# Performance work log

Hardware: AMD Instinct MI355X
Metric: run time of the kernel (lower is better)

## Reference

```python
import jax, jax.numpy as jnp
import numpy as np

N_ENT = 50000
N_REL = 200
DIM = 128
N_BASES = 4
NUM_RELATIONS = 2 * N_REL  # RGCNConv num_relations
E = 200000
S = 20000


def rgcn_conv(x, edge_index, edge_type, edge_norm, basis, att, root, bias, n_nodes):
    """RGCNConv with basis decomposition, aggr='mean'.
    x: [N, Din]; basis: [B, Din, Dout]; att: [R, B]; root: [Din, Dout]; bias: [Dout].
    """
    src, dst = edge_index[0], edge_index[1]
    x_j = x[src]                      # [E, Din] gather
    att_e = att[edge_type]            # [E, B]
    # message: x_j @ (att_e @ basis) without materializing per-edge [Din,Dout] weights
    msg = jnp.einsum('ei,bio,eb->eo', x_j, basis, att_e)  # [E, Dout]
    msg = msg * edge_norm[:, None]
    agg = jax.ops.segment_sum(msg, dst, num_segments=n_nodes)            # [N, Dout]
    cnt = jax.ops.segment_sum(jnp.ones_like(edge_norm), dst, num_segments=n_nodes)
    agg = agg / jnp.maximum(cnt, 1.0)[:, None]            # mean aggregation
    return agg + x @ root + bias


def setup_inputs() -> dict:
    key = jax.random.key(0)
    ks = jax.random.split(key, 20)
    d = {}
    d['entity'] = jnp.arange(N_ENT, dtype=jnp.int64) if jax.config.read('jax_enable_x64') else jnp.arange(N_ENT, dtype=jnp.int32)
    d['edge_index'] = jax.random.randint(ks[0], (2, E), 0, N_ENT)
    d['edge_type'] = jax.random.randint(ks[1], (E,), 0, NUM_RELATIONS)
    d['edge_norm'] = jax.random.uniform(ks[2], (E,), dtype=jnp.float32)
    d['samples'] = jax.random.randint(ks[3], (S, 3), 0, N_REL)
    d['DAD_rel'] = jax.random.normal(ks[4], (N_REL, N_REL), dtype=jnp.float32) * 0.05
    # learned parameters
    d['entity_emb'] = jax.random.normal(ks[5], (N_ENT, DIM), dtype=jnp.float32) * 0.02
    d['relation_emb'] = jax.random.normal(ks[6], (N_REL, DIM), dtype=jnp.float32) * 0.02
    d['entity_context_tab'] = jax.random.normal(ks[7], (N_ENT, DIM), dtype=jnp.float32) * 0.02
    d['relation_context_tab'] = jax.random.normal(ks[8], (N_REL, DIM), dtype=jnp.float32) * 0.02
    d['relation_gcn_weight'] = jax.random.normal(ks[9], (DIM, DIM), dtype=jnp.float32) * 0.02
    d['gate_entity'] = jax.random.uniform(ks[10], (DIM,), dtype=jnp.float32)
    d['gate_relation'] = jax.random.uniform(ks[11], (DIM,), dtype=jnp.float32)
    d['basis1'] = jax.random.normal(ks[12], (N_BASES, DIM, DIM), dtype=jnp.float32) * 0.02
    d['att1'] = jax.random.normal(ks[13], (NUM_RELATIONS, N_BASES), dtype=jnp.float32) * 0.1
    d['root1'] = jax.random.normal(ks[14], (DIM, DIM), dtype=jnp.float32) * 0.02
    d['bias1'] = jnp.zeros((DIM,), dtype=jnp.float32)
    d['basis2'] = jax.random.normal(ks[15], (N_BASES, DIM, DIM), dtype=jnp.float32) * 0.02
    d['att2'] = jax.random.normal(ks[16], (NUM_RELATIONS, N_BASES), dtype=jnp.float32) * 0.1
    d['root2'] = jax.random.normal(ks[17], (DIM, DIM), dtype=jnp.float32) * 0.02
    d['bias2'] = jnp.zeros((DIM,), dtype=jnp.float32)
    return d


def reference(entity, edge_index, edge_type, edge_norm, samples, DAD_rel,
              entity_emb, relation_emb, entity_context_tab, relation_context_tab,
              relation_gcn_weight, gate_entity, gate_relation,
              basis1, att1, root1, bias1, basis2, att2, root2, bias2):
    n_nodes = entity.shape[0]
    ent_ctx = entity_context_tab[entity]                  # [N, D]
    rel_ctx = relation_context_tab                        # arange over all relations -> full table
    ent_ctx = jax.nn.relu(rgcn_conv(ent_ctx, edge_index, edge_type, edge_norm,
                                    basis1, att1, root1, bias1, n_nodes))
    ent_ctx = jax.nn.relu(rgcn_conv(ent_ctx, edge_index, edge_type, edge_norm,
                                    basis2, att2, root2, bias2, n_nodes))
    rel_ctx = jax.nn.relu((DAD_rel @ rel_ctx) @ relation_gcn_weight)
    ge = jax.nn.sigmoid(gate_entity)
    gr = jax.nn.sigmoid(gate_relation)
    h, r, t = samples[:, 0], samples[:, 1], samples[:, 2]
    head_o = ge * entity_emb[h] + (1.0 - ge) * ent_ctx[h]
    rel_o = gr * relation_emb[r] + (1.0 - gr) * rel_ctx[r]
    tail_o = ge * entity_emb[t] + (1.0 - ge) * ent_ctx[t]
    return jnp.stack([head_o, rel_o, tail_o])             # [3, S, D]
```

## Files before the change

kernel.cpp:

```cpp
#include <hip/hip_runtime.h>
#include <hip/hip_bf16.h>

typedef short s8v  __attribute__((ext_vector_type(8)));
typedef float f16v __attribute__((ext_vector_type(16)));

__device__ __forceinline__ unsigned short f2bf(float x) {
    unsigned u = __float_as_uint(x);
    unsigned r = ((u >> 16) & 1u) + 0x7FFFu;
    return (unsigned short)((u + r) >> 16);
}
__device__ __forceinline__ float bf2f(unsigned short h) {
    return __uint_as_float(((unsigned)h) << 16);
}

__global__ __launch_bounds__(256) void x0_kernel(
    const float* __restrict__ tab, const int* __restrict__ entity,
    float* __restrict__ X0, int N)
{
    int idx = blockIdx.x * 256 + threadIdx.x;
    int n = idx >> 5, l = idx & 31;
    if (n < N) {
        int src = entity[n];
        *(float4*)&X0[(size_t)n * 128 + l * 4] =
            *(const float4*)&tab[(size_t)src * 128 + l * 4];
    }
}

__global__ __launch_bounds__(256) void bprep_kernel(
    const float* __restrict__ basis1, const float* __restrict__ root1,
    const float* __restrict__ basis2, const float* __restrict__ root2,
    unsigned short* __restrict__ Bp1h, unsigned short* __restrict__ Bp1l,
    unsigned short* __restrict__ Bp2h, unsigned short* __restrict__ Bp2l)
{
    int idx = blockIdx.x * 256 + threadIdx.x;
    int layer = blockIdx.y;
    int n = idx & 127, k = idx >> 7;
    const float* basis = layer ? basis2 : basis1;
    const float* root  = layer ? root2  : root1;
    float v = (k < 512) ? basis[((k & 3) << 14) + ((k >> 2) << 7) + n]
                        : root[((k - 512) << 7) + n];
    unsigned short h = f2bf(v);
    unsigned short l = f2bf(v - bf2f(h));
    size_t pos = (((size_t)(k >> 3) * 128) + n) * 8 + (k & 7);
    unsigned short* Bh = layer ? Bp2h : Bp1h;
    unsigned short* Bl = layer ? Bp2l : Bp1l;
    Bh[pos] = h;
    Bl[pos] = l;
}

__global__ __launch_bounds__(256) void hist_kernel(
    const int* __restrict__ edge_index, int* __restrict__ deg, int E)
{
    int e = blockIdx.x * 256 + threadIdx.x;
    if (e < E) atomicAdd(&deg[edge_index[E + e]], 1);
}

__global__ __launch_bounds__(1024) void scanA_kernel(
    const int* __restrict__ deg, int* __restrict__ row_start,
    int* __restrict__ btot, int N)
{
    __shared__ int wtot[16];
    __shared__ int woff[16];
    const int tid = threadIdx.x, lane = tid & 63, wid = tid >> 6;
    int i = blockIdx.x * 1024 + tid;
    int v = (i < N) ? deg[i] : 0;
    int x = v;
    #pragma unroll
    for (int d = 1; d < 64; d <<= 1) {
        int t = __shfl_up(x, d, 64);
        if (lane >= d) x += t;
    }
    if (lane == 63) wtot[wid] = x;
    __syncthreads();
    if (wid == 0 && lane < 16) {
        int s = wtot[lane];
        int y = s;
        #pragma unroll
        for (int d = 1; d < 16; d <<= 1) {
            int t = __shfl_up(y, d, 16);
            if (lane >= d) y += t;
        }
        woff[lane] = y - s;
        if (lane == 15) btot[blockIdx.x] = y;
    }
    __syncthreads();
    if (i < N) row_start[i] = woff[wid] + (x - v);
}

__global__ __launch_bounds__(64) void scanB_kernel(
    const int* __restrict__ btot, int* __restrict__ boff,
    int* __restrict__ row_start, int nB, int N)
{
    int t = threadIdx.x;
    int v = (t < nB) ? btot[t] : 0;
    int x = v;
    #pragma unroll
    for (int d = 1; d < 64; d <<= 1) {
        int u = __shfl_up(x, d, 64);
        if (t >= d) x += u;
    }
    if (t < nB) boff[t] = x - v;
    if (t == nB - 1) row_start[N] = x;
}

__global__ __launch_bounds__(1024) void scanC_kernel(
    int* __restrict__ row_start, int* __restrict__ cursor,
    const int* __restrict__ boff, int N)
{
    int i = blockIdx.x * 1024 + threadIdx.x;
    if (i < N) {
        int r = row_start[i] + boff[blockIdx.x];
        row_start[i] = r;
        cursor[i]    = r;
    }
}

__global__ __launch_bounds__(256) void fill_kernel(
    const int* __restrict__ edge_index, const int* __restrict__ edge_type,
    const float* __restrict__ edge_norm, int* __restrict__ cursor,
    const float* __restrict__ att1, const float* __restrict__ att2,
    int* __restrict__ src_s, float4* __restrict__ an1, float4* __restrict__ an2, int E)
{
    int e = blockIdx.x * 256 + threadIdx.x;
    if (e >= E) return;
    int dst = edge_index[E + e];
    int et  = edge_type[e];
    float n = edge_norm[e];
    int pos = atomicAdd(&cursor[dst], 1);
    src_s[pos] = edge_index[e];
    float4 a1 = *(const float4*)&att1[(size_t)et * 4];
    float4 a2 = *(const float4*)&att2[(size_t)et * 4];
    an1[pos] = make_float4(n * a1.x, n * a1.y, n * a1.z, n * a1.w);
    an2[pos] = make_float4(n * a2.x, n * a2.y, n * a2.z, n * a2.w);
}

__global__ __launch_bounds__(256) void layer_kernel(
    const float* __restrict__ X,
    const int* __restrict__ row_start,
    const int* __restrict__ src_s,
    const float4* __restrict__ an,
    const unsigned short* __restrict__ Bph,
    const unsigned short* __restrict__ Bpl,
    const float* __restrict__ bias,
    float* __restrict__ Xout, int N)
{
    __shared__ unsigned short Whi[80 * 32 * 8];
    __shared__ unsigned short Wlo[16 * 32 * 8];

    const int tid   = threadIdx.x;
    const int node0 = blockIdx.x * 32;

    {
        int g = tid >> 5, l = tid & 31;
        #pragma unroll 1
        for (int i = 0; i < 4; ++i) {
            int n  = g * 4 + i;
            int gn = node0 + n;
            float acc[4][4];
            #pragma unroll
            for (int d = 0; d < 4; ++d)
                #pragma unroll
                for (int b = 0; b < 4; ++b) acc[d][b] = 0.f;
            float inv = 1.f;
            if (gn < N) {
                int s0 = row_start[gn], s1 = row_start[gn + 1];
                for (int p = s0; p < s1; p += 4) {
                    int i1 = min(p + 1, s1 - 1);
                    int i2 = min(p + 2, s1 - 1);
                    int i3 = min(p + 3, s1 - 1);
                    int sA = src_s[p],  sB = src_s[i1];
                    int sC = src_s[i2], sD = src_s[i3];
                    float4 aA = an[p],  aB = an[i1];
                    float4 aC = an[i2], aD = an[i3];
                    if (p + 1 >= s1) aB = make_float4(0.f, 0.f, 0.f, 0.f);
                    if (p + 2 >= s1) aC = make_float4(0.f, 0.f, 0.f, 0.f);
                    if (p + 3 >= s1) aD = make_float4(0.f, 0.f, 0.f, 0.f);
                    float4 xA = *(const float4*)&X[(size_t)sA * 128 + (l << 2)];
                    float4 xB = *(const float4*)&X[(size_t)sB * 128 + (l << 2)];
                    float4 xC = *(const float4*)&X[(size_t)sC * 128 + (l << 2)];
                    float4 xD = *(const float4*)&X[(size_t)sD * 128 + (l << 2)];
                    float xsA[4] = {xA.x, xA.y, xA.z, xA.w};
                    float xsB[4] = {xB.x, xB.y, xB.z, xB.w};
                    float xsC[4] = {xC.x, xC.y, xC.z, xC.w};
                    float xsD[4] = {xD.x, xD.y, xD.z, xD.w};
                    #pragma unroll
                    for (int d = 0; d < 4; ++d) {
                        acc[d][0] = fmaf(aA.x, xsA[d], fmaf(aB.x, xsB[d], fmaf(aC.x, xsC[d], fmaf(aD.x, xsD[d], acc[d][0]))));
                        acc[d][1] = fmaf(aA.y, xsA[d], fmaf(aB.y, xsB[d], fmaf(aC.y, xsC[d], fmaf(aD.y, xsD[d], acc[d][1]))));
                        acc[d][2] = fmaf(aA.z, xsA[d], fmaf(aB.z, xsB[d], fmaf(aC.z, xsC[d], fmaf(aD.z, xsD[d], acc[d][2]))));
                        acc[d][3] = fmaf(aA.w, xsA[d], fmaf(aB.w, xsB[d], fmaf(aC.w, xsC[d], fmaf(aD.w, xsD[d], acc[d][3]))));
                    }
                }
                inv = 1.0f / fmaxf((float)(s1 - s0), 1.0f);
            }
            #pragma unroll
            for (int d = 0; d < 4; ++d) {
                int kh   = 2 * l + (d >> 1);
                int slot = n ^ (kh & 31);
                ushort4 h;
                h.x = f2bf(acc[d][0] * inv);
                h.y = f2bf(acc[d][1] * inv);
                h.z = f2bf(acc[d][2] * inv);
                h.w = f2bf(acc[d][3] * inv);
                *(ushort4*)&Whi[(kh * 32 + slot) * 8 + (d & 1) * 4] = h;
            }
        }
    }

    {
        int r  = tid >> 3;
        int kq = (tid & 7) * 16;
        int gn = node0 + r;
        float4 v0 = make_float4(0,0,0,0), v1 = v0, v2 = v0, v3 = v0;
        if (gn < N) {
            const float* xp = &X[(size_t)gn * 128 + kq];
            v0 = *(const float4*)(xp + 0);
            v1 = *(const float4*)(xp + 4);
            v2 = *(const float4*)(xp + 8);
            v3 = *(const float4*)(xp + 12);
        }
        float f[16] = {v0.x, v0.y, v0.z, v0.w, v1.x, v1.y, v1.z, v1.w,
                       v2.x, v2.y, v2.z, v2.w, v3.x, v3.y, v3.z, v3.w};
        #pragma unroll
        for (int i = 0; i < 2; ++i) {
            int kh   = 64 + (tid & 7) * 2 + i;
            int slot = r ^ (kh & 31);
            s8v h8, l8;
            #pragma unroll
            for (int j = 0; j < 8; ++j) {
                unsigned short h = f2bf(f[i * 8 + j]);
                h8[j] = (short)h;
                l8[j] = (short)f2bf(f[i * 8 + j] - bf2f(h));
            }
            *(s8v*)&Whi[(kh * 32 + slot) * 8] = h8;
            *(s8v*)&Wlo[((kh - 64) * 32 + slot) * 8] = l8;
        }
    }
    __syncthreads();

    const int lane = tid & 63, wv = tid >> 6;
    const int m    = lane & 31;
    const int kh8  = lane >> 5;
    const int c0   = wv << 5;

    f16v acc;
    #pragma unroll
    for (int i = 0; i < 16; ++i) acc[i] = 0.f;

    s8v Bb[2][8];
    auto loadB4 = [&](int g, int buf) {
        #pragma unroll
        for (int q = 0; q < 4; ++q) {
            int khg = (g * 4 + q) * 2 + kh8;
            size_t off = ((size_t)khg * 128 + c0 + m) * 8;
            Bb[buf][q * 2 + 0] = *(const s8v*)&Bph[off];
            Bb[buf][q * 2 + 1] = *(const s8v*)&Bpl[off];
        }
    };
    loadB4(0, 0);

    #pragma unroll
    for (int g = 0; g < 10; ++g) {
        int buf = g & 1;
        if (g < 9) loadB4(g + 1, buf ^ 1);
        #pragma unroll
        for (int q = 0; q < 4; ++q) {
            int s    = g * 4 + q;
            int khg  = s * 2 + kh8;
            int slot = m ^ (khg & 31);
            s8v aH = *(const s8v*)&Whi[(khg * 32 + slot) * 8];
            if (s >= 32) {
                s8v aL = *(const s8v*)&Wlo[((khg - 64) * 32 + slot) * 8];
                acc = __builtin_amdgcn_mfma_f32_32x32x16_bf16(aL, Bb[buf][q*2], acc, 0, 0, 0);
            }
            acc = __builtin_amdgcn_mfma_f32_32x32x16_bf16(aH, Bb[buf][q*2+1], acc, 0, 0, 0);
            acc = __builtin_amdgcn_mfma_f32_32x32x16_bf16(aH, Bb[buf][q*2+0], acc, 0, 0, 0);
        }
    }

    int gc = c0 + m;
    float bv = bias[gc];
    const int rbase = kh8 << 2;
    #pragma unroll
    for (int reg = 0; reg < 16; ++reg) {
        int gr = node0 + rbase + (reg & 3) + ((reg >> 2) << 3);
        if (gr < N)
            Xout[(size_t)gr * 128 + gc] = fmaxf(acc[reg] + bv, 0.f);
    }
}

__global__ __launch_bounds__(512) void relctx_kernel(
    const float* __restrict__ DAD,
    const float* __restrict__ tab,
    const float* __restrict__ W,
    float* __restrict__ R2, int NR)
{
    __shared__ float part[4][128];
    __shared__ float r1s[128];
    int r = blockIdx.x;
    int t = threadIdx.x;
    int o = t & 127, q = t >> 7;
    float s = 0.f;
    #pragma unroll 4
    for (int j = q; j < NR; j += 4)
        s = fmaf(DAD[r * NR + j], tab[j * 128 + o], s);
    part[q][o] = s;
    __syncthreads();
    if (t < 128) r1s[t] = part[0][t] + part[1][t] + part[2][t] + part[3][t];
    __syncthreads();
    float s2 = 0.f;
    #pragma unroll 8
    for (int k = q * 32; k < q * 32 + 32; ++k)
        s2 = fmaf(r1s[k], W[k * 128 + o], s2);
    part[q][o] = s2;
    __syncthreads();
    if (t < 128)
        R2[r * 128 + t] = fmaxf(part[0][t] + part[1][t] + part[2][t] + part[3][t], 0.f);
}

__global__ __launch_bounds__(256) void output_kernel(
    const int* __restrict__ samples,
    const float* __restrict__ gate_e,
    const float* __restrict__ gate_r,
    const float* __restrict__ ent_emb,
    const float* __restrict__ rel_emb,
    const float* __restrict__ ctx2,
    const float* __restrict__ relctx,
    float* __restrict__ out, int S)
{
    int s = blockIdx.x * 2 + (threadIdx.x >> 7);
    if (s >= S) return;
    int p = blockIdx.y;
    int o = threadIdx.x & 127;
    float v;
    if (p == 1) {
        int idx = samples[s * 3 + 1];
        float g = 1.0f / (1.0f + __expf(-gate_r[o]));
        v = g * rel_emb[idx * 128 + o] + (1.0f - g) * relctx[idx * 128 + o];
    } else {
        int idx = samples[s * 3 + (p == 0 ? 0 : 2)];
        float g = 1.0f / (1.0f + __expf(-gate_e[o]));
        v = g * ent_emb[(size_t)idx * 128 + o] + (1.0f - g) * ctx2[(size_t)idx * 128 + o];
    }
    out[(size_t)p * S * 128 + (size_t)s * 128 + o] = v;
}

extern "C" void kernel_launch(void* const* d_in, const int* in_sizes, int n_in,
                              void* d_out, int out_size, void* d_ws, size_t ws_size,
                              hipStream_t stream)
{
    const int*   entity     = (const int*)d_in[0];
    const int*   edge_index = (const int*)d_in[1];
    const int*   edge_type  = (const int*)d_in[2];
    const float* edge_norm  = (const float*)d_in[3];
    const int*   samples    = (const int*)d_in[4];
    const float* DAD        = (const float*)d_in[5];
    const float* ent_emb    = (const float*)d_in[6];
    const float* rel_emb    = (const float*)d_in[7];
    const float* ent_tab    = (const float*)d_in[8];
    const float* rel_tab    = (const float*)d_in[9];
    const float* Wrel       = (const float*)d_in[10];
    const float* gate_e     = (const float*)d_in[11];
    const float* gate_r     = (const float*)d_in[12];
    const float* basis1     = (const float*)d_in[13];
    const float* att1       = (const float*)d_in[14];
    const float* root1      = (const float*)d_in[15];
    const float* bias1      = (const float*)d_in[16];
    const float* basis2     = (const float*)d_in[17];
    const float* att2       = (const float*)d_in[18];
    const float* root2      = (const float*)d_in[19];
    const float* bias2      = (const float*)d_in[20];

    const int N  = in_sizes[0];
    const int E  = in_sizes[2];
    const int S  = in_sizes[4] / 3;
    const int NR = in_sizes[9] / 128;

    float* ws      = (float*)d_ws;
    float* X0      = ws;
    float* X1      = X0 + (size_t)N * 128;
    float4* an1    = (float4*)(X1 + (size_t)N * 128);
    float4* an2    = an1 + (E + 4);
    float* Rc      = (float*)(an2 + (E + 4));
    int*   deg     = (int*)(Rc + (size_t)NR * 128);
    int*   rstart  = deg + N;
    int*   cursor  = rstart + N + 1;
    int*   src_s   = cursor + N;
    int*   btot    = src_s + E + 4;
    int*   boff    = btot + 64;
    uintptr_t bt   = ((uintptr_t)(boff + 64) + 15) & ~(uintptr_t)15;
    unsigned short* Bp1h = (unsigned short*)bt;
    unsigned short* Bp1l = Bp1h + 80 * 128 * 8;
    unsigned short* Bp2h = Bp1l + 80 * 128 * 8;
    unsigned short* Bp2l = Bp2h + 80 * 128 * 8;

    const int egrid = (E + 255) / 256;
    const int lgrid = (N + 31) / 32;
    const int nB    = (N + 1023) / 1024;

    bprep_kernel<<<dim3(320, 2), 256, 0, stream>>>(basis1, root1, basis2, root2,
                                                   Bp1h, Bp1l, Bp2h, Bp2l);
    hipMemsetAsync(deg, 0, (size_t)N * sizeof(int), stream);
    hist_kernel<<<egrid, 256, 0, stream>>>(edge_index, deg, E);
    scanA_kernel<<<nB, 1024, 0, stream>>>(deg, rstart, btot, N);
    scanB_kernel<<<1, 64, 0, stream>>>(btot, boff, rstart, nB, N);
    scanC_kernel<<<nB, 1024, 0, stream>>>(rstart, cursor, boff, N);
    fill_kernel<<<egrid, 256, 0, stream>>>(edge_index, edge_type, edge_norm, cursor,
                                           att1, att2, src_s, an1, an2, E);

    x0_kernel<<<(N * 32 + 255) / 256, 256, 0, stream>>>(ent_tab, entity, X0, N);

    layer_kernel<<<lgrid, 256, 0, stream>>>(X0, rstart, src_s, an1, Bp1h, Bp1l, bias1, X1, N);

    layer_kernel<<<lgrid, 256, 0, stream>>>(X1, rstart, src_s, an2, Bp2h, Bp2l, bias2, X0, N);

    relctx_kernel<<<NR, 512, 0, stream>>>(DAD, rel_tab, Wrel, Rc, NR);

    output_kernel<<<dim3((S + 1) / 2, 3), 256, 0, stream>>>(
        samples, gate_e, gate_r, ent_emb, rel_emb, X0, Rc, (float*)d_out, S);
}
```

Measured before the change: 302.0 us.

## Store activations as split bf16 hi/lo, fuse prep kernels, interleave per-node gathers

Measured after the change: 313.1 us. +3.7%, slower.

```diff
diff --git a/kernel.cpp b/kernel.cpp
--- a/kernel.cpp
+++ b/kernel.cpp
@@ -13,46 +13,71 @@
     return __uint_as_float(((unsigned)h) << 16);
 }
 
-__global__ __launch_bounds__(256) void x0_kernel(
-    const float* __restrict__ tab, const int* __restrict__ entity,
-    float* __restrict__ X0, int N)
-{
-    int idx = blockIdx.x * 256 + threadIdx.x;
-    int n = idx >> 5, l = idx & 31;
-    if (n < N) {
-        int src = entity[n];
-        *(float4*)&X0[(size_t)n * 128 + l * 4] =
-            *(const float4*)&tab[(size_t)src * 128 + l * 4];
-    }
-}
-
-__global__ __launch_bounds__(256) void bprep_kernel(
+__global__ __launch_bounds__(256) void prep_kernel(
     const float* __restrict__ basis1, const float* __restrict__ root1,
     const float* __restrict__ basis2, const float* __restrict__ root2,
     unsigned short* __restrict__ Bp1h, unsigned short* __restrict__ Bp1l,
-    unsigned short* __restrict__ Bp2h, unsigned short* __restrict__ Bp2l)
-{
-    int idx = blockIdx.x * 256 + threadIdx.x;
-    int layer = blockIdx.y;
-    int n = idx & 127, k = idx >> 7;
-    const float* basis = layer ? basis2 : basis1;
-    const float* root  = layer ? root2  : root1;
-    float v = (k < 512) ? basis[((k & 3) << 14) + ((k >> 2) << 7) + n]
-                        : root[((k - 512) << 7) + n];
-    unsigned short h = f2bf(v);
-    unsigned short l = f2bf(v - bf2f(h));
-    size_t pos = (((size_t)(k >> 3) * 128) + n) * 8 + (k & 7);
-    unsigned short* Bh = layer ? Bp2h : Bp1h;
-    unsigned short* Bl = layer ? Bp2l : Bp1l;
-    Bh[pos] = h;
-    Bl[pos] = l;
-}
-
-__global__ __launch_bounds__(256) void hist_kernel(
-    const int* __restrict__ edge_index, int* __restrict__ deg, int E)
-{
-    int e = blockIdx.x * 256 + threadIdx.x;
-    if (e < E) atomicAdd(&deg[edge_index[E + e]], 1);
+    unsigned short* __restrict__ Bp2h, unsigned short* __restrict__ Bp2l,
+    const int* __restrict__ edge_index, int* __restrict__ deg, int E,
+    const float* __restrict__ tab, const int* __restrict__ entity,
+    unsigned short* __restrict__ X0h, unsigned short* __restrict__ X0l, int N,
+    const float* __restrict__ DAD, const float* __restrict__ rtab,
+    const float* __restrict__ Wrel, float* __restrict__ Rc, int NR)
+{
+    __shared__ float smem[384];
+    const int b = blockIdx.x, tid = threadIdx.x;
+
+    if (b < 640) {
+        int layer = b >= 320;
+        int idx = (layer ? b - 320 : b) * 256 + tid;
+        int n = idx & 127, k = idx >> 7;
+        const float* basis = layer ? basis2 : basis1;
+        const float* root  = layer ? root2  : root1;
+        float v = (k < 512) ? basis[((k & 3) << 14) + ((k >> 2) << 7) + n]
+                            : root[((k - 512) << 7) + n];
+        unsigned short h = f2bf(v);
+        unsigned short l = f2bf(v - bf2f(h));
+        size_t pos = (((size_t)(k >> 3) * 128) + n) * 8 + (k & 7);
+        (layer ? Bp2h : Bp1h)[pos] = h;
+        (layer ? Bp2l : Bp1l)[pos] = l;
+    } else if (b < 1422) {
+        int e = (b - 640) * 256 + tid;
+        if (e < E) atomicAdd(&deg[edge_index[E + e]], 1);
+    } else if (b < 7672) {
+        int idx = (b - 1422) * 256 + tid;
+        int n = idx >> 5, l = idx & 31;
+        if (n < N) {
+            int src = entity[n];
+            float4 v = *(const float4*)&tab[(size_t)src * 128 + l * 4];
+            ushort4 h, lo;
+            h.x = f2bf(v.x); lo.x = f2bf(v.x - bf2f(h.x));
+            h.y = f2bf(v.y); lo.y = f2bf(v.y - bf2f(h.y));
+            h.z = f2bf(v.z); lo.z = f2bf(v.z - bf2f(h.z));
+            h.w = f2bf(v.w); lo.w = f2bf(v.w - bf2f(h.w));
+            *(ushort4*)&X0h[(size_t)n * 128 + l * 4] = h;
+            *(ushort4*)&X0l[(size_t)n * 128 + l * 4] = lo;
+        }
+    } else {
+        float* part = smem;
+        float* r1s  = smem + 256;
+        int r = b - 7672;
+        int o = tid & 127, q = tid >> 7;
+        float s = 0.f;
+        for (int j = q; j < NR; j += 2)
+            s = fmaf(DAD[r * NR + j], rtab[j * 128 + o], s);
+        part[q * 128 + o] = s;
+        __syncthreads();
+        if (tid < 128) r1s[tid] = part[tid] + part[128 + tid];
+        __syncthreads();
+        float s2 = 0.f;
+        #pragma unroll 8
+        for (int k = q * 64; k < q * 64 + 64; ++k)
+            s2 = fmaf(r1s[k], Wrel[k * 128 + o], s2);
+        part[q * 128 + o] = s2;
+        __syncthreads();
+        if (tid < 128)
+            Rc[r * 128 + tid] = fmaxf(part[tid] + part[128 + tid], 0.f);
+    }
 }
 
 __global__ __launch_bounds__(1024) void scanA_kernel(
@@ -135,14 +160,17 @@
 }
 
 __global__ __launch_bounds__(256) void layer_kernel(
-    const float* __restrict__ X,
+    const unsigned short* __restrict__ Xh,
+    const unsigned short* __restrict__ Xl,
     const int* __restrict__ row_start,
     const int* __restrict__ src_s,
     const float4* __restrict__ an,
     const unsigned short* __restrict__ Bph,
     const unsigned short* __restrict__ Bpl,
     const float* __restrict__ bias,
-    float* __restrict__ Xout, int N)
+    unsigned short* __restrict__ Xoh,
+    unsigned short* __restrict__ Xol,
+    int N)
 {
     __shared__ unsigned short Whi[80 * 32 * 8];
     __shared__ unsigned short Wlo[16 * 32 * 8];
@@ -152,56 +180,74 @@
 
     {
         int g = tid >> 5, l = tid & 31;
-        #pragma unroll 1
+        int nb = node0 + g * 4;
+        int s0a[4], s1a[4];
+        #pragma unroll
         for (int i = 0; i < 4; ++i) {
-            int n  = g * 4 + i;
-            int gn = node0 + n;
-            float acc[4][4];
+            int gn = nb + i;
+            bool ok = gn < N;
+            s0a[i] = ok ? row_start[gn] : 0;
+            s1a[i] = ok ? row_start[gn + 1] : 0;
+        }
+        float acc[4][4][4];
+        #pragma unroll
+        for (int i = 0; i < 4; ++i)
             #pragma unroll
             for (int d = 0; d < 4; ++d)
                 #pragma unroll
-                for (int b = 0; b < 4; ++b) acc[d][b] = 0.f;
-            float inv = 1.f;
-            if (gn < N) {
-                int s0 = row_start[gn], s1 = row_start[gn + 1];
-                for (int p = s0; p < s1; p += 4) {
-                    int i1 = min(p + 1, s1 - 1);
-                    int i2 = min(p + 2, s1 - 1);
-                    int i3 = min(p + 3, s1 - 1);
-                    int sA = src_s[p],  sB = src_s[i1];
-                    int sC = src_s[i2], sD = src_s[i3];
-                    float4 aA = an[p],  aB = an[i1];
-                    float4 aC = an[i2], aD = an[i3];
-                    if (p + 1 >= s1) aB = make_float4(0.f, 0.f, 0.f, 0.f);
-                    if (p + 2 >= s1) aC = make_float4(0.f, 0.f, 0.f, 0.f);
-                    if (p + 3 >= s1) aD = make_float4(0.f, 0.f, 0.f, 0.f);
-                    float4 xA = *(const float4*)&X[(size_t)sA * 128 + (l << 2)];
-                    float4 xB = *(const float4*)&X[(size_t)sB * 128 + (l << 2)];
-                    float4 xC = *(const float4*)&X[(size_t)sC * 128 + (l << 2)];
-                    float4 xD = *(const float4*)&X[(size_t)sD * 128 + (l << 2)];
-                    float xsA[4] = {xA.x, xA.y, xA.z, xA.w};
-                    float xsB[4] = {xB.x, xB.y, xB.z, xB.w};
-                    float xsC[4] = {xC.x, xC.y, xC.z, xC.w};
-                    float xsD[4] = {xD.x, xD.y, xD.z, xD.w};
+                for (int c = 0; c < 4; ++c) acc[i][d][c] = 0.f;
+
+        int need = 0;
+        #pragma unroll
+        for (int i = 0; i < 4; ++i) need = max(need, s1a[i] - s0a[i]);
+
+        for (int p = 0; p < need; p += 4) {
+            #pragma unroll
+            for (int i = 0; i < 4; ++i) {
+                int q0 = s0a[i] + p;
+                if (q0 < s1a[i]) {
+                    int se = s1a[i] - 1;
+                    int q1 = min(q0 + 1, se);
+                    int q2 = min(q0 + 2, se);
+                    int q3 = min(q0 + 3, se);
+                    int sA = src_s[q0], sB = src_s[q1];
+                    int sC = src_s[q2], sD = src_s[q3];
+                    float4 aA = an[q0], aB = an[q1];
+                    float4 aC = an[q2], aD = an[q3];
+                    if (q0 + 1 > se) aB = make_float4(0.f, 0.f, 0.f, 0.f);
+                    if (q0 + 2 > se) aC = make_float4(0.f, 0.f, 0.f, 0.f);
+                    if (q0 + 3 > se) aD = make_float4(0.f, 0.f, 0.f, 0.f);
+                    ushort4 hA = *(const ushort4*)&Xh[(size_t)sA * 128 + (l << 2)];
+                    ushort4 hB = *(const ushort4*)&Xh[(size_t)sB * 128 + (l << 2)];
+                    ushort4 hC = *(const ushort4*)&Xh[(size_t)sC * 128 + (l << 2)];
+                    ushort4 hD = *(const ushort4*)&Xh[(size_t)sD * 128 + (l << 2)];
+                    float xsA[4] = {bf2f(hA.x), bf2f(hA.y), bf2f(hA.z), bf2f(hA.w)};
+                    float xsB[4] = {bf2f(hB.x), bf2f(hB.y), bf2f(hB.z), bf2f(hB.w)};
+                    float xsC[4] = {bf2f(hC.x), bf2f(hC.y), bf2f(hC.z), bf2f(hC.w)};
+                    float xsD[4] = {bf2f(hD.x), bf2f(hD.y), bf2f(hD.z), bf2f(hD.w)};
                     #pragma unroll
                     for (int d = 0; d < 4; ++d) {
-                        acc[d][0] = fmaf(aA.x, xsA[d], fmaf(aB.x, xsB[d], fmaf(aC.x, xsC[d], fmaf(aD.x, xsD[d], acc[d][0]))));
-                        acc[d][1] = fmaf(aA.y, xsA[d], fmaf(aB.y, xsB[d], fmaf(aC.y, xsC[d], fmaf(aD.y, xsD[d], acc[d][1]))));
-                        acc[d][2] = fmaf(aA.z, xsA[d], fmaf(aB.z, xsB[d], fmaf(aC.z, xsC[d], fmaf(aD.z, xsD[d], acc[d][2]))));
-                        acc[d][3] = fmaf(aA.w, xsA[d], fmaf(aB.w, xsB[d], fmaf(aC.w, xsC[d], fmaf(aD.w, xsD[d], acc[d][3]))));
+                        acc[i][d][0] = fmaf(aA.x, xsA[d], fmaf(aB.x, xsB[d], fmaf(aC.x, xsC[d], fmaf(aD.x, xsD[d], acc[i][d][0]))));
+                        acc[i][d][1] = fmaf(aA.y, xsA[d], fmaf(aB.y, xsB[d], fmaf(aC.y, xsC[d], fmaf(aD.y, xsD[d], acc[i][d][1]))));
+                        acc[i][d][2] = fmaf(aA.z, xsA[d], fmaf(aB.z, xsB[d], fmaf(aC.z, xsC[d], fmaf(aD.z, xsD[d], acc[i][d][2]))));
+                        acc[i][d][3] = fmaf(aA.w, xsA[d], fmaf(aB.w, xsB[d], fmaf(aC.w, xsC[d], fmaf(aD.w, xsD[d], acc[i][d][3]))));
                     }
                 }
-                inv = 1.0f / fmaxf((float)(s1 - s0), 1.0f);
             }
+        }
+        #pragma unroll
+        for (int i = 0; i < 4; ++i) {
+            int n = g * 4 + i;
+            float inv = 1.0f / fmaxf((float)(s1a[i] - s0a[i]), 1.0f);
             #pragma unroll
             for (int d = 0; d < 4; ++d) {
                 int kh   = 2 * l + (d >> 1);
                 int slot = n ^ (kh & 31);
                 ushort4 h;
-                h.x = f2bf(acc[d][0] * inv);
-                h.y = f2bf(acc[d][1] * inv);
-                h.z = f2bf(acc[d][2] * inv);
-                h.w = f2bf(acc[d][3] * inv);
+                h.x = f2bf(acc[i][d][0] * inv);
+                h.y = f2bf(acc[i][d][1] * inv);
+                h.z = f2bf(acc[i][d][2] * inv);
+                h.w = f2bf(acc[i][d][3] * inv);
                 *(ushort4*)&Whi[(kh * 32 + slot) * 8 + (d & 1) * 4] = h;
             }
         }
@@ -211,26 +257,14 @@
         int r  = tid >> 3;
         int kq = (tid & 7) * 16;
         int gn = node0 + r;
-        float4 v0 = make_float4(0,0,0,0), v1 = v0, v2 = v0, v3 = v0;
-        if (gn < N) {
-            const float* xp = &X[(size_t)gn * 128 + kq];
-            v0 = *(const float4*)(xp + 0);
-            v1 = *(const float4*)(xp + 4);
-            v2 = *(const float4*)(xp + 8);
-            v3 = *(const float4*)(xp + 12);
-        }
-        float f[16] = {v0.x, v0.y, v0.z, v0.w, v1.x, v1.y, v1.z, v1.w,
-                       v2.x, v2.y, v2.z, v2.w, v3.x, v3.y, v3.z, v3.w};
         #pragma unroll
         for (int i = 0; i < 2; ++i) {
             int kh   = 64 + (tid & 7) * 2 + i;
             int slot = r ^ (kh & 31);
-            s8v h8, l8;
-            #pragma unroll
-            for (int j = 0; j < 8; ++j) {
-                unsigned short h = f2bf(f[i * 8 + j]);
-                h8[j] = (short)h;
-                l8[j] = (short)f2bf(f[i * 8 + j] - bf2f(h));
+            s8v h8 = {0,0,0,0,0,0,0,0}, l8 = {0,0,0,0,0,0,0,0};
+            if (gn < N) {
+                h8 = *(const s8v*)&Xh[(size_t)gn * 128 + kq + i * 8];
+                l8 = *(const s8v*)&Xl[(size_t)gn * 128 + kq + i * 8];
             }
             *(s8v*)&Whi[(kh * 32 + slot) * 8] = h8;
             *(s8v*)&Wlo[((kh - 64) * 32 + slot) * 8] = l8;
@@ -284,38 +318,13 @@
     #pragma unroll
     for (int reg = 0; reg < 16; ++reg) {
         int gr = node0 + rbase + (reg & 3) + ((reg >> 2) << 3);
-        if (gr < N)
-            Xout[(size_t)gr * 128 + gc] = fmaxf(acc[reg] + bv, 0.f);
-    }
-}
-
-__global__ __launch_bounds__(512) void relctx_kernel(
-    const float* __restrict__ DAD,
-    const float* __restrict__ tab,
-    const float* __restrict__ W,
-    float* __restrict__ R2, int NR)
-{
-    __shared__ float part[4][128];
-    __shared__ float r1s[128];
-    int r = blockIdx.x;
-    int t = threadIdx.x;
-    int o = t & 127, q = t >> 7;
-    float s = 0.f;
-    #pragma unroll 4
-    for (int j = q; j < NR; j += 4)
-        s = fmaf(DAD[r * NR + j], tab[j * 128 + o], s);
-    part[q][o] = s;
-    __syncthreads();
-    if (t < 128) r1s[t] = part[0][t] + part[1][t] + part[2][t] + part[3][t];
-    __syncthreads();
-    float s2 = 0.f;
-    #pragma unroll 8
-    for (int k = q * 32; k < q * 32 + 32; ++k)
-        s2 = fmaf(r1s[k], W[k * 128 + o], s2);
-    part[q][o] = s2;
-    __syncthreads();
-    if (t < 128)
-        R2[r * 128 + t] = fmaxf(part[0][t] + part[1][t] + part[2][t] + part[3][t], 0.f);
+        if (gr < N) {
+            float v = fmaxf(acc[reg] + bv, 0.f);
+            unsigned short h = f2bf(v);
+            Xoh[(size_t)gr * 128 + gc] = h;
+            Xol[(size_t)gr * 128 + gc] = f2bf(v - bf2f(h));
+        }
+    }
 }
 
 __global__ __launch_bounds__(256) void output_kernel(
@@ -324,7 +333,8 @@
     const float* __restrict__ gate_r,
     const float* __restrict__ ent_emb,
     const float* __restrict__ rel_emb,
-    const float* __restrict__ ctx2,
+    const unsigned short* __restrict__ ctx2h,
+    const unsigned short* __restrict__ ctx2l,
     const float* __restrict__ relctx,
     float* __restrict__ out, int S)
 {
@@ -340,7 +350,8 @@
     } else {
         int idx = samples[s * 3 + (p == 0 ? 0 : 2)];
         float g = 1.0f / (1.0f + __expf(-gate_e[o]));
-        v = g * ent_emb[(size_t)idx * 128 + o] + (1.0f - g) * ctx2[(size_t)idx * 128 + o];
+        float c = bf2f(ctx2h[(size_t)idx * 128 + o]) + bf2f(ctx2l[(size_t)idx * 128 + o]);
+        v = g * ent_emb[(size_t)idx * 128 + o] + (1.0f - g) * c;
     }
     out[(size_t)p * S * 128 + (size_t)s * 128 + o] = v;
 }
@@ -376,10 +387,11 @@
     const int S  = in_sizes[4] / 3;
     const int NR = in_sizes[9] / 128;
 
-    float* ws      = (float*)d_ws;
-    float* X0      = ws;
-    float* X1      = X0 + (size_t)N * 128;
-    float4* an1    = (float4*)(X1 + (size_t)N * 128);
+    unsigned short* X0h = (unsigned short*)d_ws;
+    unsigned short* X0l = X0h + (size_t)N * 128;
+    unsigned short* X1h = X0l + (size_t)N * 128;
+    unsigned short* X1l = X1h + (size_t)N * 128;
+    float4* an1    = (float4*)(X1l + (size_t)N * 128);
     float4* an2    = an1 + (E + 4);
     float* Rc      = (float*)(an2 + (E + 4));
     int*   deg     = (int*)(Rc + (size_t)NR * 128);
@@ -397,25 +409,25 @@
     const int egrid = (E + 255) / 256;
     const int lgrid = (N + 31) / 32;
     const int nB    = (N + 1023) / 1024;
-
-    bprep_kernel<<<dim3(320, 2), 256, 0, stream>>>(basis1, root1, basis2, root2,
-                                                   Bp1h, Bp1l, Bp2h, Bp2l);
+    const int x0blocks = (N * 32 + 255) / 256;
+    const int pgrid = 640 + egrid + x0blocks + NR;
+
     hipMemsetAsync(deg, 0, (size_t)N * sizeof(int), stream);
-    hist_kernel<<<egrid, 256, 0, stream>>>(edge_index, deg, E);
+    prep_kernel<<<pgrid, 256, 0, stream>>>(
+        basis1, root1, basis2, root2, Bp1h, Bp1l, Bp2h, Bp2l,
+        edge_index, deg, E, ent_tab, entity, X0h, X0l, N,
+        DAD, rel_tab, Wrel, Rc, NR);
     scanA_kernel<<<nB, 1024, 0, stream>>>(deg, rstart, btot, N);
     scanB_kernel<<<1, 64, 0, stream>>>(btot, boff, rstart, nB, N);
     scanC_kernel<<<nB, 1024, 0, stream>>>(rstart, cursor, boff, N);
     fill_kernel<<<egrid, 256, 0, stream>>>(edge_index, edge_type, edge_norm, cursor,
                                            att1, att2, src_s, an1, an2, E);
 
-    x0_kernel<<<(N * 32 + 255) / 256, 256, 0, stream>>>(ent_tab, entity, X0, N);
-
-    layer_kernel<<<lgrid, 256, 0, stream>>>(X0, rstart, src_s, an1, Bp1h, Bp1l, bias1, X1, N);
-
-    layer_kernel<<<lgrid, 256, 0, stream>>>(X1, rstart, src_s, an2, Bp2h, Bp2l, bias2, X0, N);
-
-    relctx_kernel<<<NR, 512, 0, stream>>>(DAD, rel_tab, Wrel, Rc, NR);
+    layer_kernel<<<lgrid, 256, 0, stream>>>(X0h, X0l, rstart, src_s, an1,
+                                            Bp1h, Bp1l, bias1, X1h, X1l, N);
+    layer_kernel<<<lgrid, 256, 0, stream>>>(X1h, X1l, rstart, src_s, an2,
+                                            Bp2h, Bp2l, bias2, X0h, X0l, N);
 
     output_kernel<<<dim3((S + 1) / 2, 3), 256, 0, stream>>>(
-        samples, gate_e, gate_r, ent_emb, rel_emb, X0, Rc, (float*)d_out, S);
-}
+        samples, gate_e, gate_r, ent_emb, rel_emb, X0h, X0l, Rc, (float*)d_out, S);
+}
```
